# Performance work log

Measured on AMD Instinct MI355X. Metric: run time of the kernel, lower is better.

## Reference

```python
import jax, jax.numpy as jnp
import numpy as np

N = 100000; E = 3200000; B = 4096
F = 128; H = 128; T1 = 574; T2 = 152; MH = 128
BN_INV = float(1.0 / np.sqrt(1.0 + 1e-5))  # eval-mode BatchNorm1d, running_mean=0, running_var=1


def setup_inputs() -> dict:
    key = jax.random.key(0)
    ks = jax.random.split(key, 16)
    def w(k, shape):
        return (jax.random.normal(k, shape, jnp.float32) / np.sqrt(shape[0])).astype(jnp.float32)
    return {
        "feats": jax.random.normal(ks[0], (N, F), jnp.float32),
        "src": jax.random.randint(ks[1], (E,), 0, N, dtype=jnp.int32),
        "dst": jax.random.randint(ks[2], (E,), 0, N, dtype=jnp.int32),
        "graph_ids": jnp.sort(jax.random.randint(ks[3], (N,), 0, B, dtype=jnp.int32)),
        "W1": w(ks[4], (F, H)), "b1": jnp.zeros((H,), jnp.float32),
        "resW1": w(ks[5], (F, H)), "resb1": jnp.zeros((H,), jnp.float32),
        "W2": w(ks[6], (H, H)), "b2": jnp.zeros((H,), jnp.float32),
        "resW2": w(ks[7], (H, H)), "resb2": jnp.zeros((H,), jnp.float32),
        "aw_W": w(ks[8], (H, 1)), "aw_b": jnp.zeros((1,), jnp.float32),
        "orW1": w(ks[9], (2 * H, MH)), "orb1": jnp.zeros((MH,), jnp.float32),
        "org": jnp.ones((MH,), jnp.float32), "orbeta": jnp.zeros((MH,), jnp.float32),
        "orW2": w(ks[10], (MH, T1)), "orb2": jnp.zeros((T1,), jnp.float32),
        "scW1": w(ks[11], (2 * H + T1, MH)), "scb1": jnp.zeros((MH,), jnp.float32),
        "scg": jnp.ones((MH,), jnp.float32), "scbeta": jnp.zeros((MH,), jnp.float32),
        "scW2": w(ks[12], (MH, T2)), "scb2": jnp.zeros((T2,), jnp.float32),
    }


def _gcn_layer(feats, src, dst, W, b, resW, resb, out_norm, in_norm):
    # GraphConv with norm='both': D_out^{-1/2} on source, sum over edges, D_in^{-1/2} on dest.
    h = (feats * out_norm[:, None]) @ W                       # [N, H]
    agg = jax.ops.segment_sum(h[src], dst, num_segments=N)    # gather-compute-scatter
    out = jax.nn.relu(agg * in_norm[:, None] + b)             # activation inside GraphConv
    return out + jax.nn.relu(feats @ resW + resb)             # dgllife residual branch


def _mlp(x, Wa, ba, gam, bet, Wb, bb):
    # dgllife MLPPredictor: Dropout(0) -> Linear -> ReLU -> BatchNorm1d(eval) -> Linear
    z = jax.nn.relu(x @ Wa + ba)
    z = gam * (z * BN_INV) + bet
    return z @ Wb + bb


def _forward(feats, src, dst, graph_ids, W1, b1, resW1, resb1, W2, b2, resW2, resb2,
             aw_W, aw_b, orW1, orb1, org, orbeta, orW2, orb2,
             scW1, scb1, scg, scbeta, scW2, scb2):
    ones = jnp.ones((E,), jnp.float32)
    out_norm = jnp.clip(jax.ops.segment_sum(ones, src, num_segments=N), 1.0) ** -0.5
    in_norm = jnp.clip(jax.ops.segment_sum(ones, dst, num_segments=N), 1.0) ** -0.5
    h = _gcn_layer(feats, src, dst, W1, b1, resW1, resb1, out_norm, in_norm)
    h = _gcn_layer(h, src, dst, W2, b2, resW2, resb2, out_norm, in_norm)
    # WeightedSumAndMax readout
    aw = jax.nn.sigmoid(h @ aw_W + aw_b)                      # [N, 1] atom weights
    hsum = jax.ops.segment_sum(aw * h, graph_ids, num_segments=B)
    hmax = jax.ops.segment_max(h, graph_ids, num_segments=B)
    hmax = jnp.where(jnp.isfinite(hmax), hmax, 0.0)           # guard empty graphs
    g = jnp.concatenate([hsum, hmax], axis=1)                 # [B, 2H]
    or_logits = _mlp(g, orW1, orb1, org, orbeta, orW2, orb2)  # [B, T1]
    scent = _mlp(jnp.concatenate([g, or_logits], axis=1), scW1, scb1, scg, scbeta, scW2, scb2)
    return or_logits, scent


def reference(feats, src, dst, graph_ids, W1, b1, resW1, resb1, W2, b2, resW2, resb2,
              aw_W, aw_b, orW1, orb1, org, orbeta, orW2, orb2,
              scW1, scb1, scg, scbeta, scW2, scb2):
    return _forward(feats, src, dst, graph_ids, W1, b1, resW1, resb1, W2, b2, resW2, resb2,
                    aw_W, aw_b, orW1, orb1, org, orbeta, orW2, orb2,
                    scW1, scb1, scg, scbeta, scW2, scb2)
```

## Files before the change

kernel.cpp:

```cpp
#include <hip/hip_runtime.h>

#define NN 100000
#define EE 3200000
#define NGRAPH 4096
#define BN_INV_F 0.99999500003749981f
#define PAD 80
#define SHIFT 8
#define NBUCK 391
#define CHUNK 8192
#define NBLK 391
#define SCAN_N (2 * NBUCK * NBLK)
#define SCHUNK 2048
#define SBLKS ((SCAN_N + SCHUNK - 1) / SCHUNK)

typedef __attribute__((ext_vector_type(8))) short short8v;
typedef __attribute__((ext_vector_type(4))) float f32x4;

__device__ inline ushort f2bf(float f) {
  uint u = __builtin_bit_cast(uint, f);
  u += 0x7fff + ((u >> 16) & 1);
  return (ushort)(u >> 16);
}
__device__ inline float bf2f(ushort v) { return __builtin_bit_cast(float, (uint)v << 16); }
__device__ inline float bf_lo(uint v) { return __builtin_bit_cast(float, v << 16); }
__device__ inline float bf_hi(uint v) { return __builtin_bit_cast(float, v & 0xffff0000u); }

__global__ __launch_bounds__(256) void count_ab(const int* __restrict__ src,
                                                const int* __restrict__ dst,
                                                int* __restrict__ cnt) {
  __shared__ int hd[NBUCK], hs[NBUCK];
  int t = threadIdx.x, blk = blockIdx.x;
  for (int i = t; i < NBUCK; i += 256) { hd[i] = 0; hs[i] = 0; }
  __syncthreads();
  int base = blk * CHUNK;
#pragma unroll 4
  for (int j = 0; j < 32; j++) {
    int e = base + j * 256 + t;
    if (e < EE) {
      atomicAdd(&hd[((unsigned)dst[e]) >> SHIFT], 1);
      atomicAdd(&hs[((unsigned)src[e]) >> SHIFT], 1);
    }
  }
  __syncthreads();
  for (int i = t; i < NBUCK; i += 256) {
    cnt[i * NBLK + blk] = hd[i];
    cnt[(NBUCK + i) * NBLK + blk] = hs[i];
  }
}

__global__ __launch_bounds__(256) void scan1(const int* __restrict__ cnt,
                                             int* __restrict__ partial) {
  __shared__ int red[256];
  int b = blockIdx.x, t = threadIdx.x;
  int s = 0;
  for (int j = 0; j < 8; j++) { int i = b * SCHUNK + j * 256 + t; if (i < SCAN_N) s += cnt[i]; }
  red[t] = s;
  __syncthreads();
  for (int off = 128; off > 0; off >>= 1) {
    if (t < off) red[t] += red[t + off];
    __syncthreads();
  }
  if (t == 0) partial[b] = red[0];
}

__global__ void scan2(int* __restrict__ partial) {
  if (threadIdx.x == 0) {
    int run = 0;
    for (int i = 0; i < SBLKS; i++) { int v = partial[i]; partial[i] = run; run += v; }
  }
}

__global__ __launch_bounds__(256) void scan3(int* __restrict__ cnt,
                                             const int* __restrict__ partial) {
  __shared__ int wsum[4];
  int b = blockIdx.x, t = threadIdx.x;
  int lane = t & 63, wid = t >> 6;
  int base = b * SCHUNK + t * 8;
  int v[8];
#pragma unroll
  for (int j = 0; j < 8; j++) { int i = base + j; v[j] = (i < SCAN_N) ? cnt[i] : 0; }
  int s = ((v[0] + v[1]) + (v[2] + v[3])) + ((v[4] + v[5]) + (v[6] + v[7]));
  int inc = s;
#pragma unroll
  for (int off = 1; off < 64; off <<= 1) {
    int u = __shfl_up(inc, off);
    if (lane >= off) inc += u;
  }
  if (lane == 63) wsum[wid] = inc;
  __syncthreads();
  int woff = 0;
  for (int w = 0; w < wid; w++) woff += wsum[w];
  int excl = partial[b] + woff + (inc - s);
#pragma unroll
  for (int j = 0; j < 8; j++) {
    int i = base + j;
    if (i < SCAN_N) cnt[i] = excl;
    excl += v[j];
  }
}

__global__ __launch_bounds__(256) void scatter_c(const int* __restrict__ src,
                                                 const int* __restrict__ dst,
                                                 const int* __restrict__ off,
                                                 int2* __restrict__ ebuf,
                                                 int* __restrict__ sbuf) {
  __shared__ int cd[NBUCK], cs[NBUCK];
  int t = threadIdx.x, blk = blockIdx.x;
  for (int i = t; i < NBUCK; i += 256) {
    cd[i] = off[i * NBLK + blk];
    cs[i] = off[(NBUCK + i) * NBLK + blk] - EE;
  }
  __syncthreads();
  int base = blk * CHUNK;
#pragma unroll 4
  for (int j = 0; j < 32; j++) {
    int e = base + j * 256 + t;
    if (e < EE) {
      int d = dst[e], s = src[e];
      int p = atomicAdd(&cd[((unsigned)d) >> SHIFT], 1);
      ebuf[p] = make_int2(d, s);
      int q = atomicAdd(&cs[((unsigned)s) >> SHIFT], 1);
      sbuf[q] = s;
    }
  }
}

__global__ __launch_bounds__(256) void pass_d(const int* __restrict__ off,
                                              const int2* __restrict__ ebuf,
                                              int* __restrict__ csrp,
                                              int* __restrict__ icnt,
                                              float* __restrict__ inrm) {
  __shared__ int cur[256];
  int t = threadIdx.x, b = blockIdx.x;
  cur[t] = 0;
  __syncthreads();
  int start = off[b * NBLK];
  int end = (b == NBUCK - 1) ? EE : off[(b + 1) * NBLK];
  int node0 = b << SHIFT;
  for (int e = start + t; e < end; e += 256) {
    int2 p = ebuf[e];
    int pos = atomicAdd(&cur[p.x - node0], 1);
    if (pos < PAD) csrp[(size_t)p.x * PAD + pos] = p.y;
  }
  __syncthreads();
  int node = node0 + t;
  if (node < NN) {
    int c = cur[t];
    icnt[node] = c;
    inrm[node] = rsqrtf(fmaxf((float)c, 1.f));
  }
}

__global__ __launch_bounds__(256) void pass_d2(const int* __restrict__ off,
                                               const int* __restrict__ sbuf,
                                               float* __restrict__ onrm) {
  __shared__ int cur[256];
  int t = threadIdx.x, b = blockIdx.x;
  cur[t] = 0;
  __syncthreads();
  int start = off[(NBUCK + b) * NBLK] - EE;
  int end = (b == NBUCK - 1) ? EE : off[(NBUCK + b + 1) * NBLK] - EE;
  int node0 = b << SHIFT;
  for (int e = start + t; e < end; e += 256)
    atomicAdd(&cur[sbuf[e] - node0], 1);
  __syncthreads();
  int node = node0 + t;
  if (node < NN) onrm[node] = rsqrtf(fmaxf((float)cur[t], 1.f));
}

__global__ __launch_bounds__(256) void conv_all(
    const float* __restrict__ W1, const float* __restrict__ rW1,
    const float* __restrict__ W2, const float* __restrict__ rW2,
    const float* __restrict__ oW1, const float* __restrict__ oW2,
    const float* __restrict__ sW1, const float* __restrict__ sW2,
    ushort* __restrict__ Wt1, ushort* __restrict__ Wr1,
    ushort* __restrict__ Wt2, ushort* __restrict__ Wr2,
    ushort* __restrict__ Wm1, ushort* __restrict__ Wm2,
    ushort* __restrict__ Wm3, ushort* __restrict__ Wm4)
{
  int b = blockIdx.x;
  const float* W; ushort* O; int K, N, Kpad, c;
  if (b < 512) {
    int which = b >> 7; c = b & 127;
    K = 128; N = 128; Kpad = 128;
    W = which == 0 ? W1 : which == 1 ? rW1 : which == 2 ? W2 : rW2;
    O = which == 0 ? Wt1 : which == 1 ? Wr1 : which == 2 ? Wt2 : Wr2;
  } else if (b < 640)  { c = b - 512;  W = oW1; O = Wm1; K = 256; N = 128; Kpad = 256; }
  else if (b < 1216)   { c = b - 640;  W = oW2; O = Wm2; K = 128; N = 574; Kpad = 128; }
  else if (b < 1344)   { c = b - 1216; W = sW1; O = Wm3; K = 830; N = 128; Kpad = 832; }
  else                 { c = b - 1344; W = sW2; O = Wm4; K = 128; N = 152; Kpad = 128; }
  for (int k = threadIdx.x; k < Kpad; k += 256)
    O[(size_t)c * Kpad + k] = (c < N && k < K) ? f2bf(W[(size_t)k * N + c]) : (ushort)0;
}

template<int MODE>
__global__ __launch_bounds__(256) void gemm_mfma(
    const ushort* __restrict__ Xin, const float* __restrict__ Xf,
    ushort* __restrict__ Xbout,
    const ushort* __restrict__ Wt,
    const float* __restrict__ rowscale,
    const ushort* __restrict__ Gb, const float* __restrict__ innorm,
    const float* __restrict__ bias, const float* __restrict__ resb,
    ushort* __restrict__ outb, float* __restrict__ outf,
    const float* __restrict__ awW, const float* __restrict__ awb,
    float* __restrict__ aw)
{
  int lane = threadIdx.x & 63;
  int wid  = threadIdx.x >> 6;
  int r0   = blockIdx.x * 128 + wid * 32;
  int cl = lane & 15, kh = lane >> 4;

  short8v a[2][4];
#pragma unroll
  for (int g = 0; g < 2; g++) {
    int row  = r0 + g * 16 + cl;
    int rowc = row < NN ? row : NN - 1;
    if (MODE == 3) {
#pragma unroll
      for (int kk = 0; kk < 4; kk++) {
        const float* p = Xf + (size_t)rowc * 128 + kk * 32 + kh * 8;
        float4 v0 = *(const float4*)p;
        float4 v1 = *(const float4*)(p + 4);
        short8v t;
        t[0] = (short)f2bf(v0.x); t[1] = (short)f2bf(v0.y);
        t[2] = (short)f2bf(v0.z); t[3] = (short)f2bf(v0.w);
        t[4] = (short)f2bf(v1.x); t[5] = (short)f2bf(v1.y);
        t[6] = (short)f2bf(v1.z); t[7] = (short)f2bf(v1.w);
        a[g][kk] = t;
        if (row < NN)
          *(short8v*)(Xbout + (size_t)row * 128 + kk * 32 + kh * 8) = t;
      }
    } else {
#pragma unroll
      for (int kk = 0; kk < 4; kk++)
        a[g][kk] = *(const short8v*)(Xin + (size_t)rowc * 128 + kk * 32 + kh * 8);
    }
  }

  f32x4 acc[2][8];
#pragma unroll
  for (int g = 0; g < 2; g++)
#pragma unroll
    for (int t = 0; t < 8; t++) acc[g][t] = (f32x4){0.f, 0.f, 0.f, 0.f};

#pragma unroll
  for (int ct = 0; ct < 8; ct++) {
#pragma unroll
    for (int kk = 0; kk < 4; kk++) {
      short8v b = *(const short8v*)(Wt + (size_t)(ct * 16 + cl) * 128 + kk * 32 + kh * 8);
      acc[0][ct] = __builtin_amdgcn_mfma_f32_16x16x32_bf16(a[0][kk], b, acc[0][ct], 0, 0, 0);
      acc[1][ct] = __builtin_amdgcn_mfma_f32_16x16x32_bf16(a[1][kk], b, acc[1][ct], 0, 0, 0);
    }
  }

#pragma unroll
  for (int g = 0; g < 2; g++)
#pragma unroll
  for (int r = 0; r < 4; r++) {
    int row = r0 + g * 16 + kh * 4 + r;
    if (row >= NN) continue;
    if (MODE == 0 || MODE == 3) {
      float s = rowscale[row];
#pragma unroll
      for (int ct = 0; ct < 8; ct++)
        outb[(size_t)row * 128 + ct * 16 + cl] = f2bf(acc[g][ct][r] * s);
    } else {
      float inr = innorm[row];
      float pr = 0.f;
#pragma unroll
      for (int ct = 0; ct < 8; ct++) {
        int col = ct * 16 + cl;
        float gg  = bf2f(Gb[(size_t)row * 128 + col]) * inr + bias[col];
        float res = acc[g][ct][r] + resb[col];
        float v = fmaxf(gg, 0.f) + fmaxf(res, 0.f);
        if (MODE == 1) outb[(size_t)row * 128 + col] = f2bf(v);
        else { outf[(size_t)row * 128 + col] = v; pr += v * awW[col]; }
      }
      if (MODE == 2) {
#pragma unroll
        for (int off = 1; off < 16; off <<= 1) pr += __shfl_xor(pr, off);
        if (cl == 0) aw[row] = 1.f / (1.f + expf(-(pr + awb[0])));
      }
    }
  }
}

__global__ __launch_bounds__(256) void gather_bf16(const ushort* __restrict__ Tb,
                                                   const int* __restrict__ csrp,
                                                   const int* __restrict__ icnt,
                                                   ushort* __restrict__ Gbo) {
  int n  = blockIdx.x * 4 + (threadIdx.x >> 6);
  int c2 = threadIdx.x & 63;
  if (n >= NN) return;
  int cnt = icnt[n]; if (cnt > PAD) cnt = PAD;
  const int* row = csrp + (size_t)n * PAD;
  const uint* T32 = (const uint*)Tb;
  float a0 = 0.f, a1 = 0.f, b0 = 0.f, b1 = 0.f;
  float c0 = 0.f, c1 = 0.f, d0 = 0.f, d1 = 0.f;
  float e0 = 0.f, e1 = 0.f, f0 = 0.f, f1 = 0.f;
  float g0 = 0.f, g1 = 0.f, h0 = 0.f, h1 = 0.f;
  int j = 0;
  for (; j + 7 < cnt; j += 8) {
    int r0i = row[j],     r1i = row[j + 1], r2i = row[j + 2], r3i = row[j + 3];
    int r4i = row[j + 4], r5i = row[j + 5], r6i = row[j + 6], r7i = row[j + 7];
    uint v0 = T32[(size_t)r0i * 64 + c2];
    uint v1 = T32[(size_t)r1i * 64 + c2];
    uint v2 = T32[(size_t)r2i * 64 + c2];
    uint v3 = T32[(size_t)r3i * 64 + c2];
    uint v4 = T32[(size_t)r4i * 64 + c2];
    uint v5 = T32[(size_t)r5i * 64 + c2];
    uint v6 = T32[(size_t)r6i * 64 + c2];
    uint v7 = T32[(size_t)r7i * 64 + c2];
    a0 += bf_lo(v0); a1 += bf_hi(v0);
    b0 += bf_lo(v1); b1 += bf_hi(v1);
    c0 += bf_lo(v2); c1 += bf_hi(v2);
    d0 += bf_lo(v3); d1 += bf_hi(v3);
    e0 += bf_lo(v4); e1 += bf_hi(v4);
    f0 += bf_lo(v5); f1 += bf_hi(v5);
    g0 += bf_lo(v6); g1 += bf_hi(v6);
    h0 += bf_lo(v7); h1 += bf_hi(v7);
  }
  for (; j < cnt; j++) {
    uint v = T32[(size_t)row[j] * 64 + c2];
    a0 += bf_lo(v); a1 += bf_hi(v);
  }
  float s0 = ((a0 + b0) + (c0 + d0)) + ((e0 + f0) + (g0 + h0));
  float s1 = ((a1 + b1) + (c1 + d1)) + ((e1 + f1) + (g1 + h1));
  uint o = (uint)f2bf(s0) | ((uint)f2bf(s1) << 16);
  ((uint*)Gbo)[(size_t)n * 64 + c2] = o;
}

__global__ void readout_kernel(const float* __restrict__ h,
                               const float* __restrict__ aw,
                               const int* __restrict__ gid,
                               ushort* __restrict__ xc)
{
  int gg = blockIdx.x;
  int c  = threadIdx.x;
  int lo = 0, hi = NN;
  while (lo < hi) { int mid = (lo + hi) >> 1; if (gid[mid] < gg) lo = mid + 1; else hi = mid; }
  int start = lo;
  hi = NN;
  while (lo < hi) { int mid = (lo + hi) >> 1; if (gid[mid] < gg + 1) lo = mid + 1; else hi = mid; }
  int end = lo;
  float s = 0.f, m = 0.f;
  for (int n = start; n < end; n++) {
    float v = h[(size_t)n * 128 + c];
    s += aw[n] * v;
    m = fmaxf(m, v);
  }
  xc[(size_t)gg * 832 + c]       = f2bf(s);
  xc[(size_t)gg * 832 + 128 + c] = f2bf(m);
  if (c < 2) xc[(size_t)gg * 832 + 830 + c] = 0;
}

template<int KC1>
__global__ __launch_bounds__(256) void head_mfma(
    const ushort* __restrict__ Xb, int sx,
    const ushort* __restrict__ Wa,
    const float* __restrict__ b1v,
    const float* __restrict__ gam, const float* __restrict__ bet,
    const ushort* __restrict__ Wb,
    const float* __restrict__ b2v,
    ushort* __restrict__ outb, int sob,
    float* __restrict__ outf, int sof,
    int ncols2)
{
  __shared__ ushort zl[16][136];
  int lane = threadIdx.x & 63;
  int wid  = threadIdx.x >> 6;
  int r0   = blockIdx.x * 16;
  int cl = lane & 15, kh = lane >> 4;
  int arow = r0 + cl;

  {
    short8v a[KC1];
#pragma unroll
    for (int kk = 0; kk < KC1; kk++)
      a[kk] = *(const short8v*)(Xb + (size_t)arow * sx + kk * 32 + kh * 8);
#pragma unroll
    for (int ct = wid; ct < 8; ct += 4) {
      f32x4 acc = (f32x4){0.f, 0.f, 0.f, 0.f};
#pragma unroll
      for (int kk = 0; kk < KC1; kk++) {
        short8v b = *(const short8v*)(Wa + (size_t)(ct * 16 + cl) * (KC1 * 32) + kk * 32 + kh * 8);
        acc = __builtin_amdgcn_mfma_f32_16x16x32_bf16(a[kk], b, acc, 0, 0, 0);
      }
      int col = ct * 16 + cl;
      float bz = b1v[col], gm = gam[col], bt = bet[col];
#pragma unroll
      for (int r = 0; r < 4; r++) {
        float v = acc[r] + bz;
        v = gm * (fmaxf(v, 0.f) * BN_INV_F) + bt;
        zl[kh * 4 + r][col] = f2bf(v);
      }
    }
  }
  __syncthreads();

  short8v za[4];
#pragma unroll
  for (int kk = 0; kk < 4; kk++)
    za[kk] = *(const short8v*)&zl[cl][kk * 32 + kh * 8];

  int ntiles = (ncols2 + 15) >> 4;
  for (int ct = wid; ct < ntiles; ct += 4) {
    f32x4 acc = (f32x4){0.f, 0.f, 0.f, 0.f};
#pragma unroll
    for (int kk = 0; kk < 4; kk++) {
      short8v b = *(const short8v*)(Wb + (size_t)(ct * 16 + cl) * 128 + kk * 32 + kh * 8);
      acc = __builtin_amdgcn_mfma_f32_16x16x32_bf16(za[kk], b, acc, 0, 0, 0);
    }
    int col = ct * 16 + cl;
    if (col < ncols2) {
      float bz = b2v[col];
#pragma unroll
      for (int r = 0; r < 4; r++) {
        int row = r0 + kh * 4 + r;
        float v = acc[r] + bz;
        outf[(size_t)row * sof + col] = v;
        if (outb) outb[(size_t)row * sob + col] = f2bf(v);
      }
    }
  }
}

extern "C" void kernel_launch(void* const* d_in, const int* in_sizes, int n_in,
                              void* d_out, int out_size, void* d_ws, size_t ws_size,
                              hipStream_t stream) {
  const float* feats  = (const float*)d_in[0];
  const int*   src    = (const int*)d_in[1];
  const int*   dst    = (const int*)d_in[2];
  const int*   gid    = (const int*)d_in[3];
  const float* W1     = (const float*)d_in[4];
  const float* b1     = (const float*)d_in[5];
  const float* resW1  = (const float*)d_in[6];
  const float* resb1  = (const float*)d_in[7];
  const float* W2     = (const float*)d_in[8];
  const float* b2     = (const float*)d_in[9];
  const float* resW2  = (const float*)d_in[10];
  const float* resb2  = (const float*)d_in[11];
  const float* awW    = (const float*)d_in[12];
  const float* awb    = (const float*)d_in[13];
  const float* orW1   = (const float*)d_in[14];
  const float* orb1   = (const float*)d_in[15];
  const float* org    = (const float*)d_in[16];
  const float* orbeta = (const float*)d_in[17];
  const float* orW2   = (const float*)d_in[18];
  const float* orb2   = (const float*)d_in[19];
  const float* scW1   = (const float*)d_in[20];
  const float* scb1   = (const float*)d_in[21];
  const float* scg    = (const float*)d_in[22];
  const float* scbeta = (const float*)d_in[23];
  const float* scW2   = (const float*)d_in[24];
  const float* scb2   = (const float*)d_in[25];

  char* base = (char*)d_ws;
  ushort* Xb = (ushort*)base;
  ushort* Tb = Xb + (size_t)NN * 128;
  ushort* Lb = Tb + (size_t)NN * 128;
  float*  Hf = (float*)base;
  ushort* Gb = Lb + (size_t)NN * 128;
  int2*   ebuf = (int2*)Gb;
  int*    sbuf = (int*)Lb;
  ushort* xc  = Gb + (size_t)NN * 128;
  ushort* Wt1 = xc + (size_t)NGRAPH * 832;
  ushort* Wr1 = Wt1 + 128 * 128;
  ushort* Wt2 = Wr1 + 128 * 128;
  ushort* Wr2 = Wt2 + 128 * 128;
  ushort* Wm1 = Wr2 + 128 * 128;
  ushort* Wm2 = Wm1 + 128 * 256;
  ushort* Wm3 = Wm2 + 576 * 128;
  ushort* Wm4 = Wm3 + 128 * 832;
  float* onrm = (float*)(Wm4 + 160 * 128);
  float* inrm = onrm + NN;
  float* aw   = inrm + NN;
  int* icnt    = (int*)(aw + NN);
  int* cnt     = icnt + NN;
  int* partial = cnt + SCAN_N;
  int* csrp    = partial + SBLKS;

  float* out_or = (float*)d_out;
  float* out_sc = out_or + (size_t)NGRAPH * 574;

  count_ab<<<NBLK, 256, 0, stream>>>(src, dst, cnt);
  scan1<<<SBLKS, 256, 0, stream>>>(cnt, partial);
  scan2<<<1, 64, 0, stream>>>(partial);
  scan3<<<SBLKS, 256, 0, stream>>>(cnt, partial);
  scatter_c<<<NBLK, 256, 0, stream>>>(src, dst, cnt, ebuf, sbuf);
  pass_d<<<NBUCK, 256, 0, stream>>>(cnt, ebuf, csrp, icnt, inrm);
  pass_d2<<<NBUCK, 256, 0, stream>>>(cnt, sbuf, onrm);
  conv_all<<<1504, 256, 0, stream>>>(W1, resW1, W2, resW2, orW1, orW2, scW1, scW2,
                                     Wt1, Wr1, Wt2, Wr2, Wm1, Wm2, Wm3, Wm4);

  int gemm_grid = (NN + 127) / 128;
  gemm_mfma<3><<<gemm_grid, 256, 0, stream>>>(nullptr, feats, Xb, Wt1, onrm,
                                              nullptr, nullptr, nullptr, nullptr,
                                              Tb, nullptr, nullptr, nullptr, nullptr);
  gather_bf16<<<(NN + 3) / 4, 256, 0, stream>>>(Tb, csrp, icnt, Gb);
  gemm_mfma<1><<<gemm_grid, 256, 0, stream>>>(Xb, nullptr, nullptr, Wr1, nullptr,
                                              Gb, inrm, b1, resb1,
                                              Lb, nullptr, nullptr, nullptr, nullptr);
  gemm_mfma<0><<<gemm_grid, 256, 0, stream>>>(Lb, nullptr, nullptr, Wt2, onrm,
                                              nullptr, nullptr, nullptr, nullptr,
                                              Tb, nullptr, nullptr, nullptr, nullptr);
  gather_bf16<<<(NN + 3) / 4, 256, 0, stream>>>(Tb, csrp, icnt, Gb);
  gemm_mfma<2><<<gemm_grid, 256, 0, stream>>>(Lb, nullptr, nullptr, Wr2, nullptr,
                                              Gb, inrm, b2, resb2,
                                              nullptr, Hf, awW, awb, aw);
  readout_kernel<<<NGRAPH, 128, 0, stream>>>(Hf, aw, gid, xc);

  head_mfma<8><<<NGRAPH / 16, 256, 0, stream>>>(xc, 832, Wm1, orb1, org, orbeta,
                                                Wm2, orb2, xc + 256, 832,
                                                out_or, 574, 574);
  head_mfma<26><<<NGRAPH / 16, 256, 0, stream>>>(xc, 832, Wm3, scb1, scg, scbeta,
                                                 Wm4, scb2, nullptr, 0,
                                                 out_sc, 152, 152);
}
```

Before: 530.9 us.

## Aggregate-then-transform GCN layers fused with residual GEMM, merge head and degree kernels

Reorders each GCN layer to aggregate raw bf16 node features (scaled by the source out-norm) before multiplying by W. The gather, the transform GEMM and the residual GEMM now run in one kernel per layer, which removes the Tb and Gb intermediates and the extra launches. The two degree-pass kernels and the two MLP head kernels are each merged into one. The or-logits are kept in shared memory instead of round-tripping through global memory. The gather now reads per-edge onrm weights, and the block size shrinks to 64 rows, which may reduce how much the Wt/Wr loads are reused.

```diff
diff --git a/kernel.cpp b/kernel.cpp
--- a/kernel.cpp
+++ b/kernel.cpp
@@ -21,7 +21,6 @@
   u += 0x7fff + ((u >> 16) & 1);
   return (ushort)(u >> 16);
 }
-__device__ inline float bf2f(ushort v) { return __builtin_bit_cast(float, (uint)v << 16); }
 __device__ inline float bf_lo(uint v) { return __builtin_bit_cast(float, v << 16); }
 __device__ inline float bf_hi(uint v) { return __builtin_bit_cast(float, v & 0xffff0000u); }
 
@@ -125,47 +124,37 @@
   }
 }
 
-__global__ __launch_bounds__(256) void pass_d(const int* __restrict__ off,
-                                              const int2* __restrict__ ebuf,
-                                              int* __restrict__ csrp,
-                                              int* __restrict__ icnt,
-                                              float* __restrict__ inrm) {
-  __shared__ int cur[256];
+__global__ __launch_bounds__(256) void pass_dd(const int* __restrict__ off,
+                                               const int2* __restrict__ ebuf,
+                                               const int* __restrict__ sbuf,
+                                               int* __restrict__ csrp,
+                                               int* __restrict__ icnt,
+                                               float* __restrict__ inrm,
+                                               float* __restrict__ onrm) {
+  __shared__ int cur[256], cur2[256];
   int t = threadIdx.x, b = blockIdx.x;
-  cur[t] = 0;
-  __syncthreads();
+  cur[t] = 0; cur2[t] = 0;
+  __syncthreads();
+  int node0 = b << SHIFT;
   int start = off[b * NBLK];
   int end = (b == NBUCK - 1) ? EE : off[(b + 1) * NBLK];
-  int node0 = b << SHIFT;
   for (int e = start + t; e < end; e += 256) {
     int2 p = ebuf[e];
     int pos = atomicAdd(&cur[p.x - node0], 1);
     if (pos < PAD) csrp[(size_t)p.x * PAD + pos] = p.y;
   }
+  int s2 = off[(NBUCK + b) * NBLK] - EE;
+  int e2 = (b == NBUCK - 1) ? EE : off[(NBUCK + b + 1) * NBLK] - EE;
+  for (int e = s2 + t; e < e2; e += 256)
+    atomicAdd(&cur2[sbuf[e] - node0], 1);
   __syncthreads();
   int node = node0 + t;
   if (node < NN) {
     int c = cur[t];
     icnt[node] = c;
     inrm[node] = rsqrtf(fmaxf((float)c, 1.f));
-  }
-}
-
-__global__ __launch_bounds__(256) void pass_d2(const int* __restrict__ off,
-                                               const int* __restrict__ sbuf,
-                                               float* __restrict__ onrm) {
-  __shared__ int cur[256];
-  int t = threadIdx.x, b = blockIdx.x;
-  cur[t] = 0;
-  __syncthreads();
-  int start = off[(NBUCK + b) * NBLK] - EE;
-  int end = (b == NBUCK - 1) ? EE : off[(NBUCK + b + 1) * NBLK] - EE;
-  int node0 = b << SHIFT;
-  for (int e = start + t; e < end; e += 256)
-    atomicAdd(&cur[sbuf[e] - node0], 1);
-  __syncthreads();
-  int node = node0 + t;
-  if (node < NN) onrm[node] = rsqrtf(fmaxf((float)cur[t], 1.f));
+    onrm[node] = rsqrtf(fmaxf((float)cur2[t], 1.f));
+  }
 }
 
 __global__ __launch_bounds__(256) void conv_all(
@@ -193,141 +182,123 @@
     O[(size_t)c * Kpad + k] = (c < N && k < K) ? f2bf(W[(size_t)k * N + c]) : (ushort)0;
 }
 
+__global__ __launch_bounds__(256) void conv_x(const float* __restrict__ X,
+                                              ushort* __restrict__ Xb) {
+  int i = blockIdx.x * 256 + threadIdx.x;
+  float4 v = *(const float4*)&X[(size_t)i * 4];
+  ushort o[4] = {f2bf(v.x), f2bf(v.y), f2bf(v.z), f2bf(v.w)};
+  *(ushort4*)&Xb[(size_t)i * 4] = *(ushort4*)o;
+}
+
 template<int MODE>
-__global__ __launch_bounds__(256) void gemm_mfma(
-    const ushort* __restrict__ Xin, const float* __restrict__ Xf,
-    ushort* __restrict__ Xbout,
-    const ushort* __restrict__ Wt,
-    const float* __restrict__ rowscale,
-    const ushort* __restrict__ Gb, const float* __restrict__ innorm,
+__global__ __launch_bounds__(256) void fused_layer(
+    const ushort* __restrict__ Xg, const float* __restrict__ gscale,
+    const int* __restrict__ csrp, const int* __restrict__ icnt,
+    const ushort* __restrict__ Xr,
+    const ushort* __restrict__ Wt, const ushort* __restrict__ Wr,
+    const float* __restrict__ innorm,
     const float* __restrict__ bias, const float* __restrict__ resb,
     ushort* __restrict__ outb, float* __restrict__ outf,
     const float* __restrict__ awW, const float* __restrict__ awb,
     float* __restrict__ aw)
 {
-  int lane = threadIdx.x & 63;
-  int wid  = threadIdx.x >> 6;
-  int r0   = blockIdx.x * 128 + wid * 32;
+  __shared__ uint agg[64 * 68];
+  int t = threadIdx.x;
+  int lane = t & 63, wid = t >> 6;
+  int r0 = blockIdx.x * 64;
+  const uint* T32 = (const uint*)Xg;
+
+  for (int nn = 0; nn < 16; nn++) {
+    int node = r0 + wid * 16 + nn;
+    float a0 = 0.f, a1 = 0.f, b0 = 0.f, b1 = 0.f;
+    float c0 = 0.f, c1 = 0.f, d0 = 0.f, d1 = 0.f;
+    float e0 = 0.f, e1 = 0.f, f0 = 0.f, f1 = 0.f;
+    float g0 = 0.f, g1 = 0.f, h0 = 0.f, h1 = 0.f;
+    if (node < NN) {
+      int cnt = icnt[node]; if (cnt > PAD) cnt = PAD;
+      const int* row = csrp + (size_t)node * PAD;
+      int j = 0;
+      for (; j + 7 < cnt; j += 8) {
+        int r0i = row[j],     r1i = row[j + 1], r2i = row[j + 2], r3i = row[j + 3];
+        int r4i = row[j + 4], r5i = row[j + 5], r6i = row[j + 6], r7i = row[j + 7];
+        float w0 = gscale[r0i], w1 = gscale[r1i], w2 = gscale[r2i], w3 = gscale[r3i];
+        float w4 = gscale[r4i], w5 = gscale[r5i], w6 = gscale[r6i], w7 = gscale[r7i];
+        uint v0 = T32[(size_t)r0i * 64 + lane];
+        uint v1 = T32[(size_t)r1i * 64 + lane];
+        uint v2 = T32[(size_t)r2i * 64 + lane];
+        uint v3 = T32[(size_t)r3i * 64 + lane];
+        uint v4 = T32[(size_t)r4i * 64 + lane];
+        uint v5 = T32[(size_t)r5i * 64 + lane];
+        uint v6 = T32[(size_t)r6i * 64 + lane];
+        uint v7 = T32[(size_t)r7i * 64 + lane];
+        a0 = fmaf(w0, bf_lo(v0), a0); a1 = fmaf(w0, bf_hi(v0), a1);
+        b0 = fmaf(w1, bf_lo(v1), b0); b1 = fmaf(w1, bf_hi(v1), b1);
+        c0 = fmaf(w2, bf_lo(v2), c0); c1 = fmaf(w2, bf_hi(v2), c1);
+        d0 = fmaf(w3, bf_lo(v3), d0); d1 = fmaf(w3, bf_hi(v3), d1);
+        e0 = fmaf(w4, bf_lo(v4), e0); e1 = fmaf(w4, bf_hi(v4), e1);
+        f0 = fmaf(w5, bf_lo(v5), f0); f1 = fmaf(w5, bf_hi(v5), f1);
+        g0 = fmaf(w6, bf_lo(v6), g0); g1 = fmaf(w6, bf_hi(v6), g1);
+        h0 = fmaf(w7, bf_lo(v7), h0); h1 = fmaf(w7, bf_hi(v7), h1);
+      }
+      for (; j < cnt; j++) {
+        int ri = row[j];
+        float w = gscale[ri];
+        uint v = T32[(size_t)ri * 64 + lane];
+        a0 = fmaf(w, bf_lo(v), a0); a1 = fmaf(w, bf_hi(v), a1);
+      }
+    }
+    float s0 = ((a0 + b0) + (c0 + d0)) + ((e0 + f0) + (g0 + h0));
+    float s1 = ((a1 + b1) + (c1 + d1)) + ((e1 + f1) + (g1 + h1));
+    agg[(wid * 16 + nn) * 68 + lane] = (uint)f2bf(s0) | ((uint)f2bf(s1) << 16);
+  }
+  __syncthreads();
+
   int cl = lane & 15, kh = lane >> 4;
-
-  short8v a[2][4];
-#pragma unroll
-  for (int g = 0; g < 2; g++) {
-    int row  = r0 + g * 16 + cl;
-    int rowc = row < NN ? row : NN - 1;
-    if (MODE == 3) {
-#pragma unroll
-      for (int kk = 0; kk < 4; kk++) {
-        const float* p = Xf + (size_t)rowc * 128 + kk * 32 + kh * 8;
-        float4 v0 = *(const float4*)p;
-        float4 v1 = *(const float4*)(p + 4);
-        short8v t;
-        t[0] = (short)f2bf(v0.x); t[1] = (short)f2bf(v0.y);
-        t[2] = (short)f2bf(v0.z); t[3] = (short)f2bf(v0.w);
-        t[4] = (short)f2bf(v1.x); t[5] = (short)f2bf(v1.y);
-        t[6] = (short)f2bf(v1.z); t[7] = (short)f2bf(v1.w);
-        a[g][kk] = t;
-        if (row < NN)
-          *(short8v*)(Xbout + (size_t)row * 128 + kk * 32 + kh * 8) = t;
-      }
-    } else {
-#pragma unroll
-      for (int kk = 0; kk < 4; kk++)
-        a[g][kk] = *(const short8v*)(Xin + (size_t)rowc * 128 + kk * 32 + kh * 8);
-    }
-  }
-
-  f32x4 acc[2][8];
-#pragma unroll
-  for (int g = 0; g < 2; g++)
-#pragma unroll
-    for (int t = 0; t < 8; t++) acc[g][t] = (f32x4){0.f, 0.f, 0.f, 0.f};
-
+  short8v a1v[4], a2v[4];
+  const uint* arow = agg + (size_t)(wid * 16 + cl) * 68;
+#pragma unroll
+  for (int kk = 0; kk < 4; kk++)
+    a1v[kk] = *(const short8v*)(arow + kk * 16 + kh * 4);
+  int xrow = r0 + wid * 16 + cl; if (xrow > NN - 1) xrow = NN - 1;
+#pragma unroll
+  for (int kk = 0; kk < 4; kk++)
+    a2v[kk] = *(const short8v*)(Xr + (size_t)xrow * 128 + kk * 32 + kh * 8);
+
+  f32x4 acc1[8], acc2[8];
+#pragma unroll
+  for (int i = 0; i < 8; i++) { acc1[i] = (f32x4){0.f,0.f,0.f,0.f}; acc2[i] = acc1[i]; }
 #pragma unroll
   for (int ct = 0; ct < 8; ct++) {
 #pragma unroll
     for (int kk = 0; kk < 4; kk++) {
-      short8v b = *(const short8v*)(Wt + (size_t)(ct * 16 + cl) * 128 + kk * 32 + kh * 8);
-      acc[0][ct] = __builtin_amdgcn_mfma_f32_16x16x32_bf16(a[0][kk], b, acc[0][ct], 0, 0, 0);
-      acc[1][ct] = __builtin_amdgcn_mfma_f32_16x16x32_bf16(a[1][kk], b, acc[1][ct], 0, 0, 0);
-    }
-  }
-
-#pragma unroll
-  for (int g = 0; g < 2; g++)
+      short8v bt = *(const short8v*)(Wt + (size_t)(ct * 16 + cl) * 128 + kk * 32 + kh * 8);
+      short8v br = *(const short8v*)(Wr + (size_t)(ct * 16 + cl) * 128 + kk * 32 + kh * 8);
+      acc1[ct] = __builtin_amdgcn_mfma_f32_16x16x32_bf16(a1v[kk], bt, acc1[ct], 0, 0, 0);
+      acc2[ct] = __builtin_amdgcn_mfma_f32_16x16x32_bf16(a2v[kk], br, acc2[ct], 0, 0, 0);
+    }
+  }
+
 #pragma unroll
   for (int r = 0; r < 4; r++) {
-    int row = r0 + g * 16 + kh * 4 + r;
+    int row = r0 + wid * 16 + kh * 4 + r;
     if (row >= NN) continue;
-    if (MODE == 0 || MODE == 3) {
-      float s = rowscale[row];
-#pragma unroll
-      for (int ct = 0; ct < 8; ct++)
-        outb[(size_t)row * 128 + ct * 16 + cl] = f2bf(acc[g][ct][r] * s);
-    } else {
-      float inr = innorm[row];
-      float pr = 0.f;
-#pragma unroll
-      for (int ct = 0; ct < 8; ct++) {
-        int col = ct * 16 + cl;
-        float gg  = bf2f(Gb[(size_t)row * 128 + col]) * inr + bias[col];
-        float res = acc[g][ct][r] + resb[col];
-        float v = fmaxf(gg, 0.f) + fmaxf(res, 0.f);
-        if (MODE == 1) outb[(size_t)row * 128 + col] = f2bf(v);
-        else { outf[(size_t)row * 128 + col] = v; pr += v * awW[col]; }
-      }
-      if (MODE == 2) {
-#pragma unroll
-        for (int off = 1; off < 16; off <<= 1) pr += __shfl_xor(pr, off);
-        if (cl == 0) aw[row] = 1.f / (1.f + expf(-(pr + awb[0])));
-      }
-    }
-  }
-}
-
-__global__ __launch_bounds__(256) void gather_bf16(const ushort* __restrict__ Tb,
-                                                   const int* __restrict__ csrp,
-                                                   const int* __restrict__ icnt,
-                                                   ushort* __restrict__ Gbo) {
-  int n  = blockIdx.x * 4 + (threadIdx.x >> 6);
-  int c2 = threadIdx.x & 63;
-  if (n >= NN) return;
-  int cnt = icnt[n]; if (cnt > PAD) cnt = PAD;
-  const int* row = csrp + (size_t)n * PAD;
-  const uint* T32 = (const uint*)Tb;
-  float a0 = 0.f, a1 = 0.f, b0 = 0.f, b1 = 0.f;
-  float c0 = 0.f, c1 = 0.f, d0 = 0.f, d1 = 0.f;
-  float e0 = 0.f, e1 = 0.f, f0 = 0.f, f1 = 0.f;
-  float g0 = 0.f, g1 = 0.f, h0 = 0.f, h1 = 0.f;
-  int j = 0;
-  for (; j + 7 < cnt; j += 8) {
-    int r0i = row[j],     r1i = row[j + 1], r2i = row[j + 2], r3i = row[j + 3];
-    int r4i = row[j + 4], r5i = row[j + 5], r6i = row[j + 6], r7i = row[j + 7];
-    uint v0 = T32[(size_t)r0i * 64 + c2];
-    uint v1 = T32[(size_t)r1i * 64 + c2];
-    uint v2 = T32[(size_t)r2i * 64 + c2];
-    uint v3 = T32[(size_t)r3i * 64 + c2];
-    uint v4 = T32[(size_t)r4i * 64 + c2];
-    uint v5 = T32[(size_t)r5i * 64 + c2];
-    uint v6 = T32[(size_t)r6i * 64 + c2];
-    uint v7 = T32[(size_t)r7i * 64 + c2];
-    a0 += bf_lo(v0); a1 += bf_hi(v0);
-    b0 += bf_lo(v1); b1 += bf_hi(v1);
-    c0 += bf_lo(v2); c1 += bf_hi(v2);
-    d0 += bf_lo(v3); d1 += bf_hi(v3);
-    e0 += bf_lo(v4); e1 += bf_hi(v4);
-    f0 += bf_lo(v5); f1 += bf_hi(v5);
-    g0 += bf_lo(v6); g1 += bf_hi(v6);
-    h0 += bf_lo(v7); h1 += bf_hi(v7);
-  }
-  for (; j < cnt; j++) {
-    uint v = T32[(size_t)row[j] * 64 + c2];
-    a0 += bf_lo(v); a1 += bf_hi(v);
-  }
-  float s0 = ((a0 + b0) + (c0 + d0)) + ((e0 + f0) + (g0 + h0));
-  float s1 = ((a1 + b1) + (c1 + d1)) + ((e1 + f1) + (g1 + h1));
-  uint o = (uint)f2bf(s0) | ((uint)f2bf(s1) << 16);
-  ((uint*)Gbo)[(size_t)n * 64 + c2] = o;
+    float inr = innorm[row];
+    float pr = 0.f;
+#pragma unroll
+    for (int ct = 0; ct < 8; ct++) {
+      int col = ct * 16 + cl;
+      float g  = acc1[ct][r] * inr + bias[col];
+      float rs = acc2[ct][r] + resb[col];
+      float v = fmaxf(g, 0.f) + fmaxf(rs, 0.f);
+      if (MODE == 1) outb[(size_t)row * 128 + col] = f2bf(v);
+      else { outf[(size_t)row * 128 + col] = v; pr += v * awW[col]; }
+    }
+    if (MODE == 2) {
+#pragma unroll
+      for (int off = 1; off < 16; off <<= 1) pr += __shfl_xor(pr, off);
+      if (cl == 0) aw[row] = 1.f / (1.f + expf(-(pr + awb[0])));
+    }
+  }
 }
 
 __global__ void readout_kernel(const float* __restrict__ h,
@@ -349,24 +320,22 @@
     s += aw[n] * v;
     m = fmaxf(m, v);
   }
-  xc[(size_t)gg * 832 + c]       = f2bf(s);
-  xc[(size_t)gg * 832 + 128 + c] = f2bf(m);
-  if (c < 2) xc[(size_t)gg * 832 + 830 + c] = 0;
-}
-
-template<int KC1>
-__global__ __launch_bounds__(256) void head_mfma(
-    const ushort* __restrict__ Xb, int sx,
-    const ushort* __restrict__ Wa,
-    const float* __restrict__ b1v,
-    const float* __restrict__ gam, const float* __restrict__ bet,
-    const ushort* __restrict__ Wb,
-    const float* __restrict__ b2v,
-    ushort* __restrict__ outb, int sob,
-    float* __restrict__ outf, int sof,
-    int ncols2)
+  xc[(size_t)gg * 256 + c]       = f2bf(s);
+  xc[(size_t)gg * 256 + 128 + c] = f2bf(m);
+}
+
+__global__ __launch_bounds__(256) void head2_mfma(
+    const ushort* __restrict__ xc,
+    const ushort* __restrict__ Wm1, const float* __restrict__ orb1,
+    const float* __restrict__ org, const float* __restrict__ orbeta,
+    const ushort* __restrict__ Wm2, const float* __restrict__ orb2,
+    const ushort* __restrict__ Wm3, const float* __restrict__ scb1,
+    const float* __restrict__ scg, const float* __restrict__ scbeta,
+    const ushort* __restrict__ Wm4, const float* __restrict__ scb2,
+    float* __restrict__ out_or, float* __restrict__ out_sc)
 {
   __shared__ ushort zl[16][136];
+  __shared__ ushort lg[16][584];
   int lane = threadIdx.x & 63;
   int wid  = threadIdx.x >> 6;
   int r0   = blockIdx.x * 16;
@@ -374,52 +343,104 @@
   int arow = r0 + cl;
 
   {
-    short8v a[KC1];
-#pragma unroll
-    for (int kk = 0; kk < KC1; kk++)
-      a[kk] = *(const short8v*)(Xb + (size_t)arow * sx + kk * 32 + kh * 8);
-#pragma unroll
+    short8v a[8];
+#pragma unroll
+    for (int kk = 0; kk < 8; kk++)
+      a[kk] = *(const short8v*)(xc + (size_t)arow * 256 + kk * 32 + kh * 8);
     for (int ct = wid; ct < 8; ct += 4) {
       f32x4 acc = (f32x4){0.f, 0.f, 0.f, 0.f};
 #pragma unroll
-      for (int kk = 0; kk < KC1; kk++) {
-        short8v b = *(const short8v*)(Wa + (size_t)(ct * 16 + cl) * (KC1 * 32) + kk * 32 + kh * 8);
+      for (int kk = 0; kk < 8; kk++) {
+        short8v b = *(const short8v*)(Wm1 + (size_t)(ct * 16 + cl) * 256 + kk * 32 + kh * 8);
         acc = __builtin_amdgcn_mfma_f32_16x16x32_bf16(a[kk], b, acc, 0, 0, 0);
       }
       int col = ct * 16 + cl;
-      float bz = b1v[col], gm = gam[col], bt = bet[col];
+      float bz = orb1[col], gm = org[col], bt = orbeta[col];
 #pragma unroll
       for (int r = 0; r < 4; r++) {
         float v = acc[r] + bz;
-        v = gm * (fmaxf(v, 0.f) * BN_INV_F) + bt;
-        zl[kh * 4 + r][col] = f2bf(v);
-      }
-    }
-  }
-  __syncthreads();
-
-  short8v za[4];
-#pragma unroll
-  for (int kk = 0; kk < 4; kk++)
-    za[kk] = *(const short8v*)&zl[cl][kk * 32 + kh * 8];
-
-  int ntiles = (ncols2 + 15) >> 4;
-  for (int ct = wid; ct < ntiles; ct += 4) {
-    f32x4 acc = (f32x4){0.f, 0.f, 0.f, 0.f};
-#pragma unroll
-    for (int kk = 0; kk < 4; kk++) {
-      short8v b = *(const short8v*)(Wb + (size_t)(ct * 16 + cl) * 128 + kk * 32 + kh * 8);
-      acc = __builtin_amdgcn_mfma_f32_16x16x32_bf16(za[kk], b, acc, 0, 0, 0);
-    }
-    int col = ct * 16 + cl;
-    if (col < ncols2) {
-      float bz = b2v[col];
+        zl[kh * 4 + r][col] = f2bf(gm * (fmaxf(v, 0.f) * BN_INV_F) + bt);
+      }
+    }
+  }
+  __syncthreads();
+
+  {
+    short8v za[4];
+#pragma unroll
+    for (int kk = 0; kk < 4; kk++)
+      za[kk] = *(const short8v*)&zl[cl][kk * 32 + kh * 8];
+    for (int ct = wid; ct < 36; ct += 4) {
+      f32x4 acc = (f32x4){0.f, 0.f, 0.f, 0.f};
+#pragma unroll
+      for (int kk = 0; kk < 4; kk++) {
+        short8v b = *(const short8v*)(Wm2 + (size_t)(ct * 16 + cl) * 128 + kk * 32 + kh * 8);
+        acc = __builtin_amdgcn_mfma_f32_16x16x32_bf16(za[kk], b, acc, 0, 0, 0);
+      }
+      int col = ct * 16 + cl;
+      if (col < 574) {
+        float bz = orb2[col];
+#pragma unroll
+        for (int r = 0; r < 4; r++) {
+          int row = r0 + kh * 4 + r;
+          float v = acc[r] + bz;
+          out_or[(size_t)row * 574 + col] = v;
+          lg[kh * 4 + r][col] = f2bf(v);
+        }
+      } else {
+#pragma unroll
+        for (int r = 0; r < 4; r++) lg[kh * 4 + r][col] = 0;
+      }
+    }
+  }
+  __syncthreads();
+
+  {
+    short8v a[26];
+#pragma unroll
+    for (int kk = 0; kk < 8; kk++)
+      a[kk] = *(const short8v*)(xc + (size_t)arow * 256 + kk * 32 + kh * 8);
+#pragma unroll
+    for (int kk = 8; kk < 26; kk++)
+      a[kk] = *(const short8v*)&lg[cl][(kk - 8) * 32 + kh * 8];
+    for (int ct = wid; ct < 8; ct += 4) {
+      f32x4 acc = (f32x4){0.f, 0.f, 0.f, 0.f};
+#pragma unroll
+      for (int kk = 0; kk < 26; kk++) {
+        short8v b = *(const short8v*)(Wm3 + (size_t)(ct * 16 + cl) * 832 + kk * 32 + kh * 8);
+        acc = __builtin_amdgcn_mfma_f32_16x16x32_bf16(a[kk], b, acc, 0, 0, 0);
+      }
+      int col = ct * 16 + cl;
+      float bz = scb1[col], gm = scg[col], bt = scbeta[col];
 #pragma unroll
       for (int r = 0; r < 4; r++) {
-        int row = r0 + kh * 4 + r;
         float v = acc[r] + bz;
-        outf[(size_t)row * sof + col] = v;
-        if (outb) outb[(size_t)row * sob + col] = f2bf(v);
+        zl[kh * 4 + r][col] = f2bf(gm * (fmaxf(v, 0.f) * BN_INV_F) + bt);
+      }
+    }
+  }
+  __syncthreads();
+
+  {
+    short8v za[4];
+#pragma unroll
+    for (int kk = 0; kk < 4; kk++)
+      za[kk] = *(const short8v*)&zl[cl][kk * 32 + kh * 8];
+    for (int ct = wid; ct < 10; ct += 4) {
+      f32x4 acc = (f32x4){0.f, 0.f, 0.f, 0.f};
+#pragma unroll
+      for (int kk = 0; kk < 4; kk++) {
+        short8v b = *(const short8v*)(Wm4 + (size_t)(ct * 16 + cl) * 128 + kk * 32 + kh * 8);
+        acc = __builtin_amdgcn_mfma_f32_16x16x32_bf16(za[kk], b, acc, 0, 0, 0);
+      }
+      int col = ct * 16 + cl;
+      if (col < 152) {
+        float bz = scb2[col];
+#pragma unroll
+        for (int r = 0; r < 4; r++) {
+          int row = r0 + kh * 4 + r;
+          out_sc[(size_t)row * 152 + col] = acc[r] + bz;
+        }
       }
     }
   }
@@ -457,14 +478,12 @@
 
   char* base = (char*)d_ws;
   ushort* Xb = (ushort*)base;
-  ushort* Tb = Xb + (size_t)NN * 128;
-  ushort* Lb = Tb + (size_t)NN * 128;
-  float*  Hf = (float*)base;
-  ushort* Gb = Lb + (size_t)NN * 128;
-  int2*   ebuf = (int2*)Gb;
-  int*    sbuf = (int*)Lb;
-  ushort* xc  = Gb + (size_t)NN * 128;
-  ushort* Wt1 = xc + (size_t)NGRAPH * 832;
+  ushort* Lb = Xb + (size_t)NN * 128;
+  float*  Hf = (float*)(Lb + (size_t)NN * 128);
+  int2*   ebuf = (int2*)Hf;
+  int*    sbuf = (int*)(Hf + (size_t)NN * 64);
+  ushort* xc  = (ushort*)(Hf + (size_t)NN * 128);
+  ushort* Wt1 = xc + (size_t)NGRAPH * 256;
   ushort* Wr1 = Wt1 + 128 * 128;
   ushort* Wt2 = Wr1 + 128 * 128;
   ushort* Wr2 = Wt2 + 128 * 128;
@@ -488,32 +507,20 @@
   scan2<<<1, 64, 0, stream>>>(partial);
   scan3<<<SBLKS, 256, 0, stream>>>(cnt, partial);
   scatter_c<<<NBLK, 256, 0, stream>>>(src, dst, cnt, ebuf, sbuf);
-  pass_d<<<NBUCK, 256, 0, stream>>>(cnt, ebuf, csrp, icnt, inrm);
-  pass_d2<<<NBUCK, 256, 0, stream>>>(cnt, sbuf, onrm);
+  pass_dd<<<NBUCK, 256, 0, stream>>>(cnt, ebuf, sbuf, csrp, icnt, inrm, onrm);
   conv_all<<<1504, 256, 0, stream>>>(W1, resW1, W2, resW2, orW1, orW2, scW1, scW2,
                                      Wt1, Wr1, Wt2, Wr2, Wm1, Wm2, Wm3, Wm4);
-
-  int gemm_grid = (NN + 127) / 128;
-  gemm_mfma<3><<<gemm_grid, 256, 0, stream>>>(nullptr, feats, Xb, Wt1, onrm,
-                                              nullptr, nullptr, nullptr, nullptr,
-                                              Tb, nullptr, nullptr, nullptr, nullptr);
-  gather_bf16<<<(NN + 3) / 4, 256, 0, stream>>>(Tb, csrp, icnt, Gb);
-  gemm_mfma<1><<<gemm_grid, 256, 0, stream>>>(Xb, nullptr, nullptr, Wr1, nullptr,
-                                              Gb, inrm, b1, resb1,
-                                              Lb, nullptr, nullptr, nullptr, nullptr);
-  gemm_mfma<0><<<gemm_grid, 256, 0, stream>>>(Lb, nullptr, nullptr, Wt2, onrm,
-                                              nullptr, nullptr, nullptr, nullptr,
-                                              Tb, nullptr, nullptr, nullptr, nullptr);
-  gather_bf16<<<(NN + 3) / 4, 256, 0, stream>>>(Tb, csrp, icnt, Gb);
-  gemm_mfma<2><<<gemm_grid, 256, 0, stream>>>(Lb, nullptr, nullptr, Wr2, nullptr,
-                                              Gb, inrm, b2, resb2,
-                                              nullptr, Hf, awW, awb, aw);
+  conv_x<<<12500, 256, 0, stream>>>(feats, Xb);
+
+  int grid = (NN + 63) / 64;
+  fused_layer<1><<<grid, 256, 0, stream>>>(Xb, onrm, csrp, icnt, Xb, Wt1, Wr1,
+                                           inrm, b1, resb1, Lb, nullptr,
+                                           nullptr, nullptr, nullptr);
+  fused_layer<2><<<grid, 256, 0, stream>>>(Lb, onrm, csrp, icnt, Lb, Wt2, Wr2,
+                                           inrm, b2, resb2, nullptr, Hf,
+                                           awW, awb, aw);
   readout_kernel<<<NGRAPH, 128, 0, stream>>>(Hf, aw, gid, xc);
-
-  head_mfma<8><<<NGRAPH / 16, 256, 0, stream>>>(xc, 832, Wm1, orb1, org, orbeta,
-                                                Wm2, orb2, xc + 256, 832,
-                                                out_or, 574, 574);
-  head_mfma<26><<<NGRAPH / 16, 256, 0, stream>>>(xc, 832, Wm3, scb1, scg, scbeta,
-                                                 Wm4, scb2, nullptr, 0,
-                                                 out_sc, 152, 152);
-}
+  head2_mfma<<<NGRAPH / 16, 256, 0, stream>>>(xc, Wm1, orb1, org, orbeta, Wm2, orb2,
+                                              Wm3, scb1, scg, scbeta, Wm4, scb2,
+                                              out_or, out_sc);
+}
```

New measurement: 660.7 us. 24.5% more time.
